# Optimization experiments

Hardware: AMD Instinct MI355X
Metric: run time of the kernel (lower is better)

Reference implementation:

```python
import jax, jax.numpy as jnp
import numpy as np

VOCAB, D, H, L, SEQ = 32000, 768, 12, 6, 1024
HD = D // H
DFF = 4 * D
EPS = 1e-5


def _ln(x, g, b):
    mu = jnp.mean(x, axis=-1, keepdims=True)
    var = jnp.var(x, axis=-1, keepdims=True)
    return (x - mu) * jax.lax.rsqrt(var + EPS) * g + b


def setup_inputs() -> dict:
    key = jax.random.key(0)
    ks = jax.random.split(key, 10)
    s = lambda *sh: 0.02
    return {
        "idx": jax.random.randint(ks[0], (2, SEQ), 0, VOCAB, dtype=jnp.int64) if jax.config.jax_enable_x64 else jax.random.randint(ks[0], (2, SEQ), 0, VOCAB, dtype=jnp.int32),
        "tok_emb": jax.random.normal(ks[1], (VOCAB, D), jnp.float32) * 0.02,
        "pos_emb": jax.random.normal(ks[2], (SEQ, D), jnp.float32) * 0.02,
        "Wqkv": jax.random.normal(ks[3], (L, D, 3 * D), jnp.float32) * 0.02,
        "bqkv": jnp.zeros((L, 3 * D), jnp.float32),
        "Wo": jax.random.normal(ks[4], (L, D, D), jnp.float32) * 0.02,
        "bo": jnp.zeros((L, D), jnp.float32),
        "ln1_g": jnp.ones((L, D), jnp.float32),
        "ln1_b": jnp.zeros((L, D), jnp.float32),
        "ln2_g": jnp.ones((L, D), jnp.float32),
        "ln2_b": jnp.zeros((L, D), jnp.float32),
        "W1": jax.random.normal(ks[5], (L, D, DFF), jnp.float32) * 0.02,
        "b1": jnp.zeros((L, DFF), jnp.float32),
        "W2": jax.random.normal(ks[6], (L, DFF, D), jnp.float32) * 0.02,
        "b2": jnp.zeros((L, D), jnp.float32),
        "lnf_g": jnp.ones((D,), jnp.float32),
        "lnf_b": jnp.zeros((D,), jnp.float32),
        "Wlm": jax.random.normal(ks[7], (D, VOCAB), jnp.float32) * 0.02,
    }


def _forward(idx, tok_emb, pos_emb, Wqkv, bqkv, Wo, bo, ln1_g, ln1_b,
             ln2_g, ln2_b, W1, b1, W2, b2, lnf_g, lnf_b, Wlm):
    B, T = idx.shape
    x = tok_emb[idx] + pos_emb[None, :T]  # [B,T,D]
    causal = jnp.tril(jnp.ones((T, T), bool))  # [T,T]
    for l in range(L):
        h = _ln(x, ln1_g[l], ln1_b[l])
        qkv = h @ Wqkv[l] + bqkv[l]  # [B,T,3D]
        qkv = qkv.reshape(B, T, 3, H, HD).transpose(2, 0, 3, 1, 4)
        q, k, v = qkv[0], qkv[1], qkv[2]  # each [B,H,T,HD]
        att = jnp.einsum('bhqd,bhkd->bhqk', q, k) / np.sqrt(HD).astype(np.float32)
        att = jnp.where(causal, att, -jnp.inf)
        att = jax.nn.softmax(att, axis=-1)
        o = jnp.einsum('bhqk,bhkd->bhqd', att, v)
        o = o.transpose(0, 2, 1, 3).reshape(B, T, D)
        x = x + o @ Wo[l] + bo[l]
        h = _ln(x, ln2_g[l], ln2_b[l])
        x = x + jax.nn.gelu(h @ W1[l] + b1[l], approximate=False) @ W2[l] + b2[l]
    x = _ln(x, lnf_g, lnf_b)
    return x @ Wlm  # [B,T,VOCAB]


def reference(idx, tok_emb, pos_emb, Wqkv, bqkv, Wo, bo, ln1_g, ln1_b,
              ln2_g, ln2_b, W1, b1, W2, b2, lnf_g, lnf_b, Wlm):
    return _forward(idx, tok_emb, pos_emb, Wqkv, bqkv, Wo, bo, ln1_g, ln1_b,
                    ln2_g, ln2_b, W1, b1, W2, b2, lnf_g, lnf_b, Wlm)
```

## Files before the change

kernel.cpp:

```cpp
#include <hip/hip_runtime.h>
#include <math.h>

#define TT   1024
#define DD   768
#define HH   12
#define LLAY 6
#define DFFN 3072
#define BB   2
#define NTOK (BB*TT)

typedef __bf16 bf16;
typedef __attribute__((ext_vector_type(8))) __bf16 bf16x8;
typedef __attribute__((ext_vector_type(4))) __bf16 bf16x4;
typedef __attribute__((ext_vector_type(4))) float f32x4;

__device__ inline unsigned pack_bf16x2(float a, float b) {
    union { bf16 h[2]; unsigned u; } un;
    un.h[0] = (bf16)a; un.h[1] = (bf16)b;
    return un.u;
}

__device__ inline void gload16(const bf16* g, bf16* l) {
    __builtin_amdgcn_global_load_lds((const void*)g, (void*)l, 16, 0, 0);
}

template<int N> __device__ inline void waitcnt_vm() {
    if constexpr (N == 0) asm volatile("s_waitcnt vmcnt(0)" ::: "memory");
    else if constexpr (N == 3) asm volatile("s_waitcnt vmcnt(3)" ::: "memory");
    else if constexpr (N == 4) asm volatile("s_waitcnt vmcnt(4)" ::: "memory");
}

__global__ __launch_bounds__(256) void embed_kernel(const int* __restrict__ idx,
                                                    const float* __restrict__ tok,
                                                    const float* __restrict__ pos,
                                                    float* __restrict__ x) {
    int bt = blockIdx.x;
    int t  = bt % TT;
    int id = idx[bt];
    const float* te = tok + (size_t)id * DD;
    const float* pe = pos + (size_t)t * DD;
    float* xr = x + (size_t)bt * DD;
    for (int d = threadIdx.x; d < DD; d += 256) xr[d] = te[d] + pe[d];
}

__global__ __launch_bounds__(256) void ln_kernel(const float* __restrict__ in,
                                                 const float* __restrict__ g,
                                                 const float* __restrict__ b,
                                                 bf16* __restrict__ out) {
    int row = blockIdx.x;
    const float* xr = in + (size_t)row * DD;
    float s = 0.f, s2 = 0.f;
    for (int d = threadIdx.x; d < DD; d += 256) { float v = xr[d]; s += v; s2 += v * v; }
    for (int off = 32; off; off >>= 1) { s += __shfl_down(s, off); s2 += __shfl_down(s2, off); }
    __shared__ float aS[4], aS2[4];
    __shared__ float mu_s, rs_s;
    int wid = threadIdx.x >> 6, lane = threadIdx.x & 63;
    if (lane == 0) { aS[wid] = s; aS2[wid] = s2; }
    __syncthreads();
    if (threadIdx.x == 0) {
        float t1 = aS[0] + aS[1] + aS[2] + aS[3];
        float t2 = aS2[0] + aS2[1] + aS2[2] + aS2[3];
        float mu = t1 / (float)DD;
        float var = t2 / (float)DD - mu * mu;
        mu_s = mu; rs_s = rsqrtf(var + 1e-5f);
    }
    __syncthreads();
    float mu = mu_s, rs = rs_s;
    bf16* orow = out + (size_t)row * DD;
    for (int d = threadIdx.x; d < DD; d += 256)
        orow[d] = (bf16)((xr[d] - mu) * rs * g[d] + b[d]);
}

__device__ inline void convT_tile(const float* __restrict__ in, bf16* __restrict__ out,
                                  int K, int N, int k0, int n0) {
    __shared__ float tile[32][33];
    int tn = threadIdx.x & 31, tk = threadIdx.x >> 5;
#pragma unroll
    for (int i = 0; i < 4; ++i)
        tile[tk + i * 8][tn] = in[(size_t)(k0 + tk + i * 8) * N + n0 + tn];
    __syncthreads();
#pragma unroll
    for (int i = 0; i < 4; ++i)
        out[(size_t)(n0 + tk + i * 8) * K + k0 + tn] = (bf16)tile[tn][tk + i * 8];
}

__global__ __launch_bounds__(256) void convT_kernel(const float* __restrict__ in,
                                                    bf16* __restrict__ out,
                                                    int K, int N) {
    convT_tile(in, out, K, N, blockIdx.y * 32, blockIdx.x * 32);
}

__global__ __launch_bounds__(256) void convT4_kernel(const float* __restrict__ w0,
                                                     const float* __restrict__ w1,
                                                     const float* __restrict__ w2,
                                                     const float* __restrict__ w3,
                                                     bf16* __restrict__ o0,
                                                     bf16* __restrict__ o1,
                                                     bf16* __restrict__ o2,
                                                     bf16* __restrict__ o3) {
    int bid = blockIdx.x;
    const float* in; bf16* out; int K, N, t;
    if (bid < 1728)      { in = w0; out = o0; K = 768;  N = 2304; t = bid; }
    else if (bid < 2304) { in = w1; out = o1; K = 768;  N = 768;  t = bid - 1728; }
    else if (bid < 4608) { in = w2; out = o2; K = 768;  N = 3072; t = bid - 2304; }
    else                 { in = w3; out = o3; K = 3072; N = 768;  t = bid - 4608; }
    int nt = N / 32;
    convT_tile(in, out, K, N, (t / nt) * 32, (t % nt) * 32);
}

template<int BM, int EPI>
__global__ __launch_bounds__(256) void mgemm(const bf16* __restrict__ A,
                                             const bf16* __restrict__ Bt,
                                             const float* __restrict__ bias,
                                             const float* __restrict__ res,
                                             void* __restrict__ Cout,
                                             bf16* __restrict__ vtout,
                                             int M, int N, int K) {
    constexpr int MF = BM / 32;
    constexpr int NF = 4;
    constexpr int AIT = BM / 64;
    constexpr int STG = AIT + 2;
    constexpr int ASZ = BM * 32;
    constexpr int BUFE = ASZ + 128 * 32;
    __shared__ __align__(16) bf16 smem[3 * BUFE];
    int bm = blockIdx.y * BM;
    int bn = blockIdx.x * 128;
    int tid = threadIdx.x;
    int lane = tid & 63;
    int w = tid >> 6;
    int wr = w >> 1, wc = w & 1;
    int l15 = lane & 15, g = lane >> 4;

    f32x4 acc[MF][NF];
#pragma unroll
    for (int m = 0; m < MF; ++m)
#pragma unroll
        for (int n = 0; n < NF; ++n) acc[m][n] = (f32x4){0.f, 0.f, 0.f, 0.f};

    int r = lane >> 2;
    int koff = ((lane & 3) ^ ((r >> 1) & 3)) * 8;
    const bf16* Ab = A + (size_t)(bm + w * 16 + r) * K + koff;
    const bf16* Bb = Bt + (size_t)(bn + w * 16 + r) * K + koff;

    auto stage = [&](int p, int k0) {
        bf16* base = smem + p * BUFE;
        bf16* Asb = base + w * 16 * 32;
        bf16* Bsb = base + ASZ + w * 16 * 32;
#pragma unroll
        for (int it = 0; it < AIT; ++it)
            gload16(Ab + (size_t)(it * 64) * K + k0, Asb + it * 64 * 32);
#pragma unroll
        for (int it = 0; it < 2; ++it)
            gload16(Bb + (size_t)(it * 64) * K + k0, Bsb + it * 64 * 32);
    };

    stage(0, 0);
    stage(1, 32);
    waitcnt_vm<STG>();
    __builtin_amdgcn_s_barrier();
    int cur = 0;

    for (int k0 = 0; k0 < K; k0 += 32) {
        const bf16* Ac = smem + cur * BUFE;
        const bf16* Bc = Ac + ASZ;
        bf16x8 af[MF], bfv[NF];
#pragma unroll
        for (int m = 0; m < MF; ++m) {
            int row = wr * (BM / 2) + m * 16 + l15;
            int gs = g ^ ((row >> 1) & 3);
            af[m] = *(const bf16x8*)&Ac[row * 32 + gs * 8];
        }
#pragma unroll
        for (int n = 0; n < NF; ++n) {
            int row = wc * 64 + n * 16 + l15;
            int gs = g ^ ((row >> 1) & 3);
            bfv[n] = *(const bf16x8*)&Bc[row * 32 + gs * 8];
        }
        bool st = (k0 + 64 < K);
        if (st) {
            int nxt = cur + 2; if (nxt >= 3) nxt -= 3;
            stage(nxt, k0 + 64);
        }
#pragma unroll
        for (int m = 0; m < MF; ++m)
#pragma unroll
            for (int n = 0; n < NF; ++n)
                acc[m][n] = __builtin_amdgcn_mfma_f32_16x16x32_bf16(af[m], bfv[n], acc[m][n], 0, 0, 0);
        if (st) waitcnt_vm<STG>();
        else    waitcnt_vm<0>();
        __builtin_amdgcn_s_barrier();
        cur = (cur == 2) ? 0 : cur + 1;
    }

    int lq = g * 4;
#pragma unroll
    for (int m = 0; m < MF; ++m) {
#pragma unroll
        for (int n = 0; n < NF; ++n) {
            int col = bn + wc * 64 + n * 16 + l15;
            float bv = bias[col];
            if (EPI == 4 && col >= 2 * DD) {
                int row0 = bm + wr * (BM / 2) + m * 16 + lq;
                int b = row0 >> 10, t0 = row0 & 1023;
                int hd = col - 2 * DD;
                union { bf16 h[4]; unsigned long long u; } pk;
#pragma unroll
                for (int j = 0; j < 4; ++j) pk.h[j] = (bf16)(acc[m][n][j] + bv);
                *(unsigned long long*)&vtout[((size_t)(b * DD + hd)) * TT + t0] = pk.u;
            } else {
#pragma unroll
                for (int j = 0; j < 4; ++j) {
                    int row = bm + wr * (BM / 2) + m * 16 + lq + j;
                    float v = acc[m][n][j] + bv;
                    if (EPI == 2) {
                        ((float*)Cout)[(size_t)row * N + col] = v + res[(size_t)row * N + col];
                    } else if (EPI == 3) {
                        v = 0.5f * v * (1.f + erff(v * 0.70710678118654752f));
                        ((bf16*)Cout)[(size_t)row * N + col] = (bf16)v;
                    } else if (EPI == 1) {
                        ((bf16*)Cout)[(size_t)row * N + col] = (bf16)v;
                    } else {
                        if (col < DD) v *= 0.125f;
                        ((bf16*)Cout)[(size_t)row * N + col] = (bf16)v;
                    }
                }
            }
        }
    }
}

__global__ __launch_bounds__(512, 2) void lmgemm(const bf16* __restrict__ A,
                                                 const bf16* __restrict__ Bt,
                                                 float* __restrict__ C) {
    constexpr int BUFE = 2 * 256 * 64;
    __shared__ __align__(16) bf16 smem[2 * BUFE];
    const int tid = threadIdx.x;
    const int w = tid >> 6, lane = tid & 63;
    const int wm = w >> 2, wn = w & 3;
    const int l15 = lane & 15, g = lane >> 4;
    const int bm = blockIdx.x * 256;
    const int bn = blockIdx.y * 256;

    const int swzr = (l15 >> 1) & 7;
    const int pc0 = (g ^ swzr) * 8;

    const int r8 = lane >> 3, c8 = lane & 7;
    const bf16* agp[4]; const bf16* bgp[4];
    int aldso[4], bldso[4];
#pragma unroll
    for (int j = 0; j < 4; ++j) {
        int br = w * 32 + j * 8 + r8;
        int swz = (br >> 1) & 7;
        agp[j] = A  + (size_t)(bm + br) * DD + (c8 ^ swz) * 8;
        bgp[j] = Bt + (size_t)(bn + br) * DD + (c8 ^ swz) * 8;
        aldso[j] = (w * 32 + j * 8) * 64;
        bldso[j] = 256 * 64 + (w * 32 + j * 8) * 64;
    }

    f32x4 acc[8][4];
#pragma unroll
    for (int m = 0; m < 8; ++m)
#pragma unroll
        for (int n = 0; n < 4; ++n) acc[m][n] = (f32x4){0.f, 0.f, 0.f, 0.f};

    {
        bf16* base = smem;
#pragma unroll
        for (int j = 0; j < 4; ++j) gload16(agp[j], base + aldso[j]);
#pragma unroll
        for (int j = 0; j < 4; ++j) gload16(bgp[j], base + bldso[j]);
    }
    __syncthreads();
    int cur = 0;

    for (int t = 0; t < 12; ++t) {
        const bf16* Ar = smem + cur * BUFE;
        const bf16* Br = Ar + 256 * 64;
        bf16* nbase = smem + (cur ^ 1) * BUFE;
        const int k0n = (t + 1) * 64;
        const bool st = (t < 11);
        if (st) {
#pragma unroll
            for (int j = 0; j < 4; ++j) gload16(agp[j] + k0n, nbase + aldso[j]);
        }
        bf16x8 af[8], bfv[4];
#pragma unroll
        for (int m = 0; m < 8; ++m)
            af[m] = *(const bf16x8*)&Ar[(wm * 128 + m * 16 + l15) * 64 + pc0];
#pragma unroll
        for (int n = 0; n < 4; ++n)
            bfv[n] = *(const bf16x8*)&Br[(wn * 64 + n * 16 + l15) * 64 + pc0];
        __builtin_amdgcn_s_setprio(1);
#pragma unroll
        for (int m = 0; m < 8; ++m)
#pragma unroll
            for (int n = 0; n < 4; ++n)
                acc[m][n] = __builtin_amdgcn_mfma_f32_16x16x32_bf16(af[m], bfv[n], acc[m][n], 0, 0, 0);
        __builtin_amdgcn_s_setprio(0);
        if (st) {
#pragma unroll
            for (int j = 0; j < 4; ++j) gload16(bgp[j] + k0n, nbase + bldso[j]);
        }
#pragma unroll
        for (int m = 0; m < 8; ++m)
            af[m] = *(const bf16x8*)&Ar[(wm * 128 + m * 16 + l15) * 64 + (pc0 ^ 32)];
#pragma unroll
        for (int n = 0; n < 4; ++n)
            bfv[n] = *(const bf16x8*)&Br[(wn * 64 + n * 16 + l15) * 64 + (pc0 ^ 32)];
        __builtin_amdgcn_s_setprio(1);
#pragma unroll
        for (int m = 0; m < 8; ++m)
#pragma unroll
            for (int n = 0; n < 4; ++n)
                acc[m][n] = __builtin_amdgcn_mfma_f32_16x16x32_bf16(af[m], bfv[n], acc[m][n], 0, 0, 0);
        __builtin_amdgcn_s_setprio(0);
        __syncthreads();
        cur ^= 1;
    }

    float* eb = (float*)smem + w * (16 * 68);
    const int rr = lane >> 2, c0 = (lane & 3) * 16;
#pragma unroll
    for (int mf = 0; mf < 8; ++mf) {
#pragma unroll
        for (int n = 0; n < 4; ++n)
#pragma unroll
            for (int j = 0; j < 4; ++j)
                eb[(g * 4 + j) * 68 + n * 16 + l15] = acc[mf][n][j];
        __syncthreads();
        const float* src = &eb[rr * 68 + c0];
        float* dst = C + (size_t)(bm + wm * 128 + mf * 16 + rr) * 32000 + bn + wn * 64 + c0;
        *(float4*)(dst + 0)  = *(const float4*)(src + 0);
        *(float4*)(dst + 4)  = *(const float4*)(src + 4);
        *(float4*)(dst + 8)  = *(const float4*)(src + 8);
        *(float4*)(dst + 12) = *(const float4*)(src + 12);
        __syncthreads();
    }
}

__global__ __launch_bounds__(256) void fattn_kernel(const bf16* __restrict__ qkv,
                                                    const bf16* __restrict__ vt,
                                                    bf16* __restrict__ o) {
    const int bh = blockIdx.y;
    const int b = bh / HH, h = bh % HH;
    const int q0 = blockIdx.x * 64;
    const int tid = threadIdx.x;
    const int w = tid >> 6, lane = tid & 63;
    const int l15 = lane & 15, g = lane >> 4;

    __shared__ __align__(16) bf16 Ks[64 * 64];
    __shared__ __align__(16) bf16 Vs[64 * 64];
    __shared__ __align__(16) bf16 Ps[4][16 * 64];

    const size_t basebt = (size_t)b * TT;
    const int qw = q0 + w * 16;
    const int qg = qw + l15;

    bf16x8 bq0, bq1;
    {
        const bf16* qp = qkv + (basebt + qw + l15) * 2304 + h * 64 + g * 8;
        bq0 = *(const bf16x8*)(qp);
        bq1 = *(const bf16x8*)(qp + 32);
    }

    float mstate = -1e30f, lstate = 0.f;
    f32x4 oacc[4];
#pragma unroll
    for (int nf = 0; nf < 4; ++nf) oacc[nf] = (f32x4){0.f, 0.f, 0.f, 0.f};

    const int swzA = (l15 & 7) << 4;
    char* const psBase = (char*)&Ps[w][0];

    const int nchunk = blockIdx.x + 1;
    for (int c = 0; c < nchunk; ++c) {
        const int kc = c * 64;
        __syncthreads();
        {
            int r0 = tid >> 3;
            int e0 = (tid & 7) * 8;
#pragma unroll
            for (int i = 0; i < 2; ++i) {
                int r = r0 + 32 * i;
                int swzW = (r & 7) << 4;
                bf16x8 kv = *(const bf16x8*)&qkv[(basebt + kc + r) * 2304 + DD + h * 64 + e0];
                *(bf16x8*)((char*)Ks + r * 128 + ((e0 * 2) ^ swzW)) = kv;
                bf16x8 vv = *(const bf16x8*)&vt[((size_t)bh * 64 + r) * TT + kc + e0];
                *(bf16x8*)((char*)Vs + r * 128 + ((e0 * 2) ^ swzW)) = vv;
            }
        }
        __syncthreads();
        if (kc > qw + 15) continue;

        f32x4 s[4];
        __builtin_amdgcn_s_setprio(1);
#pragma unroll
        for (int mf = 0; mf < 4; ++mf) {
            char* kr = (char*)Ks + (16 * mf + l15) * 128;
            bf16x8 ka0 = *(const bf16x8*)(kr + ((16 * g) ^ swzA));
            bf16x8 ka1 = *(const bf16x8*)(kr + ((64 + 16 * g) ^ swzA));
            f32x4 a = (f32x4){0.f, 0.f, 0.f, 0.f};
            a = __builtin_amdgcn_mfma_f32_16x16x32_bf16(ka0, bq0, a, 0, 0, 0);
            a = __builtin_amdgcn_mfma_f32_16x16x32_bf16(ka1, bq1, a, 0, 0, 0);
            s[mf] = a;
        }
        __builtin_amdgcn_s_setprio(0);
        if (kc + 63 > qw) {
#pragma unroll
            for (int mf = 0; mf < 4; ++mf)
#pragma unroll
                for (int j = 0; j < 4; ++j)
                    if (kc + 16 * mf + 4 * g + j > qg) s[mf][j] = -1e30f;
        }
        float cm = -1e30f;
#pragma unroll
        for (int mf = 0; mf < 4; ++mf)
#pragma unroll
            for (int j = 0; j < 4; ++j) cm = fmaxf(cm, s[mf][j]);
        cm = fmaxf(cm, __shfl_xor(cm, 16));
        cm = fmaxf(cm, __shfl_xor(cm, 32));
        float mnew = fmaxf(mstate, cm);
        float sc = __expf(mstate - mnew);
        mstate = mnew;
        float p[4][4];
        float psum = 0.f;
#pragma unroll
        for (int mf = 0; mf < 4; ++mf)
#pragma unroll
            for (int j = 0; j < 4; ++j) { float pv = __expf(s[mf][j] - mnew); p[mf][j] = pv; psum += pv; }
        psum += __shfl_xor(psum, 16);
        psum += __shfl_xor(psum, 32);
        lstate = lstate * sc + psum;
#pragma unroll
        for (int mf = 0; mf < 4; ++mf) {
            unsigned lo = pack_bf16x2(p[mf][0], p[mf][1]);
            unsigned hi = pack_bf16x2(p[mf][2], p[mf][3]);
            char* dst = psBase + l15 * 128 + ((32 * mf + 8 * g) ^ swzA);
            *(unsigned*)dst = lo;
            *(unsigned*)(dst + 4) = hi;
        }
        float s0 = __shfl(sc, 4 * g + 0), s1 = __shfl(sc, 4 * g + 1);
        float s2 = __shfl(sc, 4 * g + 2), s3 = __shfl(sc, 4 * g + 3);
#pragma unroll
        for (int nf = 0; nf < 4; ++nf) {
            oacc[nf][0] *= s0; oacc[nf][1] *= s1; oacc[nf][2] *= s2; oacc[nf][3] *= s3;
        }
        bf16x8 pa0 = *(const bf16x8*)(psBase + l15 * 128 + ((16 * g) ^ swzA));
        bf16x8 pa1 = *(const bf16x8*)(psBase + l15 * 128 + ((64 + 16 * g) ^ swzA));
        __builtin_amdgcn_s_setprio(1);
#pragma unroll
        for (int nf = 0; nf < 4; ++nf) {
            char* vr = (char*)Vs + (16 * nf + l15) * 128;
            bf16x8 vb0 = *(const bf16x8*)(vr + ((16 * g) ^ swzA));
            bf16x8 vb1 = *(const bf16x8*)(vr + ((64 + 16 * g) ^ swzA));
            oacc[nf] = __builtin_amdgcn_mfma_f32_16x16x32_bf16(pa0, vb0, oacc[nf], 0, 0, 0);
            oacc[nf] = __builtin_amdgcn_mfma_f32_16x16x32_bf16(pa1, vb1, oacc[nf], 0, 0, 0);
        }
        __builtin_amdgcn_s_setprio(0);
    }
    float linv = 1.f / lstate;
    float l0 = __shfl(linv, 4 * g + 0), l1 = __shfl(linv, 4 * g + 1);
    float l2 = __shfl(linv, 4 * g + 2), l3 = __shfl(linv, 4 * g + 3);
    float lj[4] = {l0, l1, l2, l3};
#pragma unroll
    for (int j = 0; j < 4; ++j) {
        bf16* orow = o + (size_t)(basebt + qw + 4 * g + j) * DD + h * 64 + l15;
#pragma unroll
        for (int nf = 0; nf < 4; ++nf)
            orow[16 * nf] = (bf16)(oacc[nf][j] * lj[j]);
    }
}

extern "C" void kernel_launch(void* const* d_in, const int* in_sizes, int n_in,
                              void* d_out, int out_size, void* d_ws, size_t ws_size,
                              hipStream_t stream) {
    (void)in_sizes; (void)n_in; (void)out_size; (void)ws_size;
    const int*   idx  = (const int*)d_in[0];
    const float* tok  = (const float*)d_in[1];
    const float* pos  = (const float*)d_in[2];
    const float* Wqkv = (const float*)d_in[3];
    const float* bqkv = (const float*)d_in[4];
    const float* Wo   = (const float*)d_in[5];
    const float* bo   = (const float*)d_in[6];
    const float* ln1g = (const float*)d_in[7];
    const float* ln1b = (const float*)d_in[8];
    const float* ln2g = (const float*)d_in[9];
    const float* ln2b = (const float*)d_in[10];
    const float* W1   = (const float*)d_in[11];
    const float* b1   = (const float*)d_in[12];
    const float* W2   = (const float*)d_in[13];
    const float* b2   = (const float*)d_in[14];
    const float* lnfg = (const float*)d_in[15];
    const float* lnfb = (const float*)d_in[16];
    const float* Wlm  = (const float*)d_in[17];
    float* out = (float*)d_out;

    char* ws = (char*)d_ws;
    float* x     = (float*)(ws);
    bf16*  abuf0 = (bf16*)(ws + 6291456);
    bf16*  abuf1 = (bf16*)(ws + 9437184);
    bf16*  qkvb  = (bf16*)(ws + 22020096);
    bf16*  vtb   = (bf16*)(ws + 31457280);
    bf16*  wbuf  = (bf16*)(ws + 34603008);

    bf16* wq = wbuf;
    bf16* wo = wbuf + 1769472;
    bf16* w1 = wbuf + 2359296;
    bf16* w2 = wbuf + 4718592;

    embed_kernel<<<NTOK, 256, 0, stream>>>(idx, tok, pos, x);

    for (int l = 0; l < LLAY; ++l) {
        convT4_kernel<<<6912, 256, 0, stream>>>(
            Wqkv + (size_t)l * DD * 3 * DD, Wo + (size_t)l * DD * DD,
            W1 + (size_t)l * DD * DFFN, W2 + (size_t)l * DFFN * DD,
            wq, wo, w1, w2);
        ln_kernel<<<NTOK, 256, 0, stream>>>(x, ln1g + l * DD, ln1b + l * DD, abuf0);
        mgemm<128, 4><<<dim3(3 * DD / 128, NTOK / 128), 256, 0, stream>>>(
            abuf0, wq, bqkv + (size_t)l * 3 * DD, nullptr, qkvb, vtb, NTOK, 3 * DD, DD);
        fattn_kernel<<<dim3(TT / 64, BB * HH), 256, 0, stream>>>(qkvb, vtb, abuf0);
        mgemm<64, 2><<<dim3(DD / 128, NTOK / 64), 256, 0, stream>>>(
            abuf0, wo, bo + (size_t)l * DD, x, x, nullptr, NTOK, DD, DD);
        ln_kernel<<<NTOK, 256, 0, stream>>>(x, ln2g + l * DD, ln2b + l * DD, abuf0);
        mgemm<128, 3><<<dim3(DFFN / 128, NTOK / 128), 256, 0, stream>>>(
            abuf0, w1, b1 + (size_t)l * DFFN, nullptr, abuf1, nullptr, NTOK, DFFN, DD);
        mgemm<64, 2><<<dim3(DD / 128, NTOK / 64), 256, 0, stream>>>(
            abuf1, w2, b2 + (size_t)l * DD, x, x, nullptr, NTOK, DD, DFFN);
    }
    ln_kernel<<<NTOK, 256, 0, stream>>>(x, lnfg, lnfb, abuf0);
    convT_kernel<<<dim3(32000 / 32, DD / 32), 256, 0, stream>>>(Wlm, wbuf, DD, 32000);
    lmgemm<<<dim3(NTOK / 256, 32000 / 256), 512, 0, stream>>>(abuf0, wbuf, out);
}
```

Before: 1.008 ms.

## Deepen LM-head GEMM pipeline, wave-per-row layernorm, reverse attention block order

The LM-head GEMM moves from a two-buffer pipeline with K-step 64 to a four-buffer pipeline with K-step 32. Three stages stay in flight, gated by vmcnt waits and raw barriers, so global-to-LDS loads overlap the MFMA work. Layernorm now gives each wavefront one row, using float4 loads and a shuffle reduction in place of shared-memory block reductions and syncthreads. Flash attention launches the longest causal query blocks first to balance load across the tail. The deeper pipeline uses more LDS and changes the swizzle, which could affect occupancy or cause bank conflicts.

```diff
diff --git a/kernel.cpp b/kernel.cpp
--- a/kernel.cpp
+++ b/kernel.cpp
@@ -28,6 +28,7 @@
     if constexpr (N == 0) asm volatile("s_waitcnt vmcnt(0)" ::: "memory");
     else if constexpr (N == 3) asm volatile("s_waitcnt vmcnt(3)" ::: "memory");
     else if constexpr (N == 4) asm volatile("s_waitcnt vmcnt(4)" ::: "memory");
+    else if constexpr (N == 8) asm volatile("s_waitcnt vmcnt(8)" ::: "memory");
 }
 
 __global__ __launch_bounds__(256) void embed_kernel(const int* __restrict__ idx,
@@ -47,28 +48,33 @@
                                                  const float* __restrict__ g,
                                                  const float* __restrict__ b,
                                                  bf16* __restrict__ out) {
-    int row = blockIdx.x;
+    const int wid = threadIdx.x >> 6, lane = threadIdx.x & 63;
+    const int row = blockIdx.x * 4 + wid;
     const float* xr = in + (size_t)row * DD;
+    float4 v[3];
     float s = 0.f, s2 = 0.f;
-    for (int d = threadIdx.x; d < DD; d += 256) { float v = xr[d]; s += v; s2 += v * v; }
+#pragma unroll
+    for (int j = 0; j < 3; ++j) {
+        v[j] = *(const float4*)&xr[lane * 4 + 256 * j];
+        s  += v[j].x + v[j].y + v[j].z + v[j].w;
+        s2 += v[j].x * v[j].x + v[j].y * v[j].y + v[j].z * v[j].z + v[j].w * v[j].w;
+    }
     for (int off = 32; off; off >>= 1) { s += __shfl_down(s, off); s2 += __shfl_down(s2, off); }
-    __shared__ float aS[4], aS2[4];
-    __shared__ float mu_s, rs_s;
-    int wid = threadIdx.x >> 6, lane = threadIdx.x & 63;
-    if (lane == 0) { aS[wid] = s; aS2[wid] = s2; }
-    __syncthreads();
-    if (threadIdx.x == 0) {
-        float t1 = aS[0] + aS[1] + aS[2] + aS[3];
-        float t2 = aS2[0] + aS2[1] + aS2[2] + aS2[3];
-        float mu = t1 / (float)DD;
-        float var = t2 / (float)DD - mu * mu;
-        mu_s = mu; rs_s = rsqrtf(var + 1e-5f);
-    }
-    __syncthreads();
-    float mu = mu_s, rs = rs_s;
+    s = __shfl(s, 0); s2 = __shfl(s2, 0);
+    const float mu = s / (float)DD;
+    const float rs = rsqrtf(s2 / (float)DD - mu * mu + 1e-5f);
     bf16* orow = out + (size_t)row * DD;
-    for (int d = threadIdx.x; d < DD; d += 256)
-        orow[d] = (bf16)((xr[d] - mu) * rs * g[d] + b[d]);
+#pragma unroll
+    for (int j = 0; j < 3; ++j) {
+        float4 gg = *(const float4*)&g[lane * 4 + 256 * j];
+        float4 bb = *(const float4*)&b[lane * 4 + 256 * j];
+        bf16x4 o;
+        o[0] = (bf16)((v[j].x - mu) * rs * gg.x + bb.x);
+        o[1] = (bf16)((v[j].y - mu) * rs * gg.y + bb.y);
+        o[2] = (bf16)((v[j].z - mu) * rs * gg.z + bb.z);
+        o[3] = (bf16)((v[j].w - mu) * rs * gg.w + bb.w);
+        *(bf16x4*)&orow[lane * 4 + 256 * j] = o;
+    }
 }
 
 __device__ inline void convT_tile(const float* __restrict__ in, bf16* __restrict__ out,
@@ -232,8 +238,9 @@
 __global__ __launch_bounds__(512, 2) void lmgemm(const bf16* __restrict__ A,
                                                  const bf16* __restrict__ Bt,
                                                  float* __restrict__ C) {
-    constexpr int BUFE = 2 * 256 * 64;
-    __shared__ __align__(16) bf16 smem[2 * BUFE];
+    constexpr int ABUF = 256 * 32;
+    constexpr int BUFE = 2 * ABUF;
+    __shared__ __align__(16) bf16 smem[4 * BUFE];
     const int tid = threadIdx.x;
     const int w = tid >> 6, lane = tid & 63;
     const int wm = w >> 2, wn = w & 3;
@@ -241,21 +248,14 @@
     const int bm = blockIdx.x * 256;
     const int bn = blockIdx.y * 256;
 
-    const int swzr = (l15 >> 1) & 7;
-    const int pc0 = (g ^ swzr) * 8;
-
-    const int r8 = lane >> 3, c8 = lane & 7;
-    const bf16* agp[4]; const bf16* bgp[4];
-    int aldso[4], bldso[4];
-#pragma unroll
-    for (int j = 0; j < 4; ++j) {
-        int br = w * 32 + j * 8 + r8;
-        int swz = (br >> 1) & 7;
-        agp[j] = A  + (size_t)(bm + br) * DD + (c8 ^ swz) * 8;
-        bgp[j] = Bt + (size_t)(bn + br) * DD + (c8 ^ swz) * 8;
-        aldso[j] = (w * 32 + j * 8) * 64;
-        bldso[j] = 256 * 64 + (w * 32 + j * 8) * 64;
-    }
+    const int fcol = ((g ^ ((l15 >> 1) & 3))) * 8;
+
+    const int rA = lane >> 2;
+    const int csw = ((lane & 3) ^ ((lane >> 3) & 3)) * 8;
+    const bf16* a0 = A  + (size_t)(bm + w * 16 + rA) * DD + csw;
+    const bf16* b0 = Bt + (size_t)(bn + w * 16 + rA) * DD + csw;
+    const int ld0 = (w * 16) * 32;
+    const int ld1 = (w * 16 + 128) * 32;
 
     f32x4 acc[8][4];
 #pragma unroll
@@ -263,33 +263,31 @@
 #pragma unroll
         for (int n = 0; n < 4; ++n) acc[m][n] = (f32x4){0.f, 0.f, 0.f, 0.f};
 
-    {
-        bf16* base = smem;
-#pragma unroll
-        for (int j = 0; j < 4; ++j) gload16(agp[j], base + aldso[j]);
-#pragma unroll
-        for (int j = 0; j < 4; ++j) gload16(bgp[j], base + bldso[j]);
-    }
-    __syncthreads();
-    int cur = 0;
-
-    for (int t = 0; t < 12; ++t) {
-        const bf16* Ar = smem + cur * BUFE;
-        const bf16* Br = Ar + 256 * 64;
-        bf16* nbase = smem + (cur ^ 1) * BUFE;
-        const int k0n = (t + 1) * 64;
-        const bool st = (t < 11);
-        if (st) {
-#pragma unroll
-            for (int j = 0; j < 4; ++j) gload16(agp[j] + k0n, nbase + aldso[j]);
-        }
+    auto stagef = [&](int p, int kelem) {
+        bf16* base = smem + p * BUFE;
+        gload16(a0 + kelem, base + ld0);
+        gload16(a0 + (size_t)128 * DD + kelem, base + ld1);
+        gload16(b0 + kelem, base + ABUF + ld0);
+        gload16(b0 + (size_t)128 * DD + kelem, base + ABUF + ld1);
+    };
+
+    stagef(0, 0);
+    stagef(1, 32);
+    stagef(2, 64);
+    waitcnt_vm<8>();
+    __builtin_amdgcn_s_barrier();
+
+    for (int t = 0; t < 21; ++t) {
+        const bf16* Ar = smem + (t & 3) * BUFE;
+        const bf16* Br = Ar + ABUF;
         bf16x8 af[8], bfv[4];
 #pragma unroll
         for (int m = 0; m < 8; ++m)
-            af[m] = *(const bf16x8*)&Ar[(wm * 128 + m * 16 + l15) * 64 + pc0];
+            af[m] = *(const bf16x8*)&Ar[(wm * 128 + m * 16 + l15) * 32 + fcol];
 #pragma unroll
         for (int n = 0; n < 4; ++n)
-            bfv[n] = *(const bf16x8*)&Br[(wn * 64 + n * 16 + l15) * 64 + pc0];
+            bfv[n] = *(const bf16x8*)&Br[(wn * 64 + n * 16 + l15) * 32 + fcol];
+        stagef((t + 3) & 3, (t + 3) * 32);
         __builtin_amdgcn_s_setprio(1);
 #pragma unroll
         for (int m = 0; m < 8; ++m)
@@ -297,27 +295,30 @@
             for (int n = 0; n < 4; ++n)
                 acc[m][n] = __builtin_amdgcn_mfma_f32_16x16x32_bf16(af[m], bfv[n], acc[m][n], 0, 0, 0);
         __builtin_amdgcn_s_setprio(0);
-        if (st) {
-#pragma unroll
-            for (int j = 0; j < 4; ++j) gload16(bgp[j] + k0n, nbase + bldso[j]);
-        }
+        waitcnt_vm<8>();
+        __builtin_amdgcn_s_barrier();
+    }
+    waitcnt_vm<0>();
+    __builtin_amdgcn_s_barrier();
+#pragma unroll
+    for (int t = 21; t < 24; ++t) {
+        const bf16* Ar = smem + (t & 3) * BUFE;
+        const bf16* Br = Ar + ABUF;
+        bf16x8 af[8], bfv[4];
 #pragma unroll
         for (int m = 0; m < 8; ++m)
-            af[m] = *(const bf16x8*)&Ar[(wm * 128 + m * 16 + l15) * 64 + (pc0 ^ 32)];
+            af[m] = *(const bf16x8*)&Ar[(wm * 128 + m * 16 + l15) * 32 + fcol];
 #pragma unroll
         for (int n = 0; n < 4; ++n)
-            bfv[n] = *(const bf16x8*)&Br[(wn * 64 + n * 16 + l15) * 64 + (pc0 ^ 32)];
-        __builtin_amdgcn_s_setprio(1);
+            bfv[n] = *(const bf16x8*)&Br[(wn * 64 + n * 16 + l15) * 32 + fcol];
 #pragma unroll
         for (int m = 0; m < 8; ++m)
 #pragma unroll
             for (int n = 0; n < 4; ++n)
                 acc[m][n] = __builtin_amdgcn_mfma_f32_16x16x32_bf16(af[m], bfv[n], acc[m][n], 0, 0, 0);
-        __builtin_amdgcn_s_setprio(0);
-        __syncthreads();
-        cur ^= 1;
-    }
-
+    }
+
+    __syncthreads();
     float* eb = (float*)smem + w * (16 * 68);
     const int rr = lane >> 2, c0 = (lane & 3) * 16;
 #pragma unroll
@@ -343,7 +344,8 @@
                                                     bf16* __restrict__ o) {
     const int bh = blockIdx.y;
     const int b = bh / HH, h = bh % HH;
-    const int q0 = blockIdx.x * 64;
+    const int qc = gridDim.x - 1 - blockIdx.x;
+    const int q0 = qc * 64;
     const int tid = threadIdx.x;
     const int w = tid >> 6, lane = tid & 63;
     const int l15 = lane & 15, g = lane >> 4;
@@ -371,7 +373,7 @@
     const int swzA = (l15 & 7) << 4;
     char* const psBase = (char*)&Ps[w][0];
 
-    const int nchunk = blockIdx.x + 1;
+    const int nchunk = qc + 1;
     for (int c = 0; c < nchunk; ++c) {
         const int kc = c * 64;
         __syncthreads();
@@ -514,19 +516,19 @@
             Wqkv + (size_t)l * DD * 3 * DD, Wo + (size_t)l * DD * DD,
             W1 + (size_t)l * DD * DFFN, W2 + (size_t)l * DFFN * DD,
             wq, wo, w1, w2);
-        ln_kernel<<<NTOK, 256, 0, stream>>>(x, ln1g + l * DD, ln1b + l * DD, abuf0);
+        ln_kernel<<<NTOK / 4, 256, 0, stream>>>(x, ln1g + l * DD, ln1b + l * DD, abuf0);
         mgemm<128, 4><<<dim3(3 * DD / 128, NTOK / 128), 256, 0, stream>>>(
             abuf0, wq, bqkv + (size_t)l * 3 * DD, nullptr, qkvb, vtb, NTOK, 3 * DD, DD);
         fattn_kernel<<<dim3(TT / 64, BB * HH), 256, 0, stream>>>(qkvb, vtb, abuf0);
         mgemm<64, 2><<<dim3(DD / 128, NTOK / 64), 256, 0, stream>>>(
             abuf0, wo, bo + (size_t)l * DD, x, x, nullptr, NTOK, DD, DD);
-        ln_kernel<<<NTOK, 256, 0, stream>>>(x, ln2g + l * DD, ln2b + l * DD, abuf0);
+        ln_kernel<<<NTOK / 4, 256, 0, stream>>>(x, ln2g + l * DD, ln2b + l * DD, abuf0);
         mgemm<128, 3><<<dim3(DFFN / 128, NTOK / 128), 256, 0, stream>>>(
             abuf0, w1, b1 + (size_t)l * DFFN, nullptr, abuf1, nullptr, NTOK, DFFN, DD);
         mgemm<64, 2><<<dim3(DD / 128, NTOK / 64), 256, 0, stream>>>(
             abuf1, w2, b2 + (size_t)l * DD, x, x, nullptr, NTOK, DD, DFFN);
     }
-    ln_kernel<<<NTOK, 256, 0, stream>>>(x, lnfg, lnfb, abuf0);
+    ln_kernel<<<NTOK / 4, 256, 0, stream>>>(x, lnfg, lnfb, abuf0);
     convT_kernel<<<dim3(32000 / 32, DD / 32), 256, 0, stream>>>(Wlm, wbuf, DD, 32000);
     lmgemm<<<dim3(NTOK / 256, 32000 / 256), 512, 0, stream>>>(abuf0, wbuf, out);
 }
```

Result: no change. 1.005 ms (-0.3%).

## Vectorize layernorm per-wave, enlarge transpose tiles, remap LM-head blocks, reverse attention order

Applied to the files above, without the earlier changes.

Layernorm now handles one row per wavefront with float4 loads and shuffle reductions, removing shared-memory reductions and block syncs. Weight transposes use 64x64 tiles with fewer blocks. The LM-head GEMM uses a 1D grid remapped so each XCD processes contiguous vocab column blocks for L2 reuse, with out-of-range blocks exiting early. Causal attention launches the heaviest query blocks first to reduce tail imbalance.

```diff
diff --git a/kernel.cpp b/kernel.cpp
--- a/kernel.cpp
+++ b/kernel.cpp
@@ -47,47 +47,52 @@
                                                  const float* __restrict__ g,
                                                  const float* __restrict__ b,
                                                  bf16* __restrict__ out) {
-    int row = blockIdx.x;
+    const int wid = threadIdx.x >> 6, lane = threadIdx.x & 63;
+    const int row = blockIdx.x * 4 + wid;
     const float* xr = in + (size_t)row * DD;
+    float4 v[3];
     float s = 0.f, s2 = 0.f;
-    for (int d = threadIdx.x; d < DD; d += 256) { float v = xr[d]; s += v; s2 += v * v; }
+#pragma unroll
+    for (int j = 0; j < 3; ++j) {
+        v[j] = *(const float4*)&xr[lane * 4 + 256 * j];
+        s  += v[j].x + v[j].y + v[j].z + v[j].w;
+        s2 += v[j].x * v[j].x + v[j].y * v[j].y + v[j].z * v[j].z + v[j].w * v[j].w;
+    }
     for (int off = 32; off; off >>= 1) { s += __shfl_down(s, off); s2 += __shfl_down(s2, off); }
-    __shared__ float aS[4], aS2[4];
-    __shared__ float mu_s, rs_s;
-    int wid = threadIdx.x >> 6, lane = threadIdx.x & 63;
-    if (lane == 0) { aS[wid] = s; aS2[wid] = s2; }
+    s = __shfl(s, 0); s2 = __shfl(s2, 0);
+    const float mu = s / (float)DD;
+    const float rs = rsqrtf(s2 / (float)DD - mu * mu + 1e-5f);
+    bf16* orow = out + (size_t)row * DD;
+#pragma unroll
+    for (int j = 0; j < 3; ++j) {
+        float4 gg = *(const float4*)&g[lane * 4 + 256 * j];
+        float4 bb = *(const float4*)&b[lane * 4 + 256 * j];
+        bf16x4 o;
+        o[0] = (bf16)((v[j].x - mu) * rs * gg.x + bb.x);
+        o[1] = (bf16)((v[j].y - mu) * rs * gg.y + bb.y);
+        o[2] = (bf16)((v[j].z - mu) * rs * gg.z + bb.z);
+        o[3] = (bf16)((v[j].w - mu) * rs * gg.w + bb.w);
+        *(bf16x4*)&orow[lane * 4 + 256 * j] = o;
+    }
+}
+
+__device__ inline void convT_tile64(const float* __restrict__ in, bf16* __restrict__ out,
+                                    int K, int N, int k0, int n0) {
+    __shared__ float tile[64][65];
+    const int c = threadIdx.x & 63, q = threadIdx.x >> 6;
+#pragma unroll
+    for (int i = 0; i < 16; ++i)
+        tile[q + i * 4][c] = in[(size_t)(k0 + q + i * 4) * N + n0 + c];
     __syncthreads();
-    if (threadIdx.x == 0) {
-        float t1 = aS[0] + aS[1] + aS[2] + aS[3];
-        float t2 = aS2[0] + aS2[1] + aS2[2] + aS2[3];
-        float mu = t1 / (float)DD;
-        float var = t2 / (float)DD - mu * mu;
-        mu_s = mu; rs_s = rsqrtf(var + 1e-5f);
-    }
-    __syncthreads();
-    float mu = mu_s, rs = rs_s;
-    bf16* orow = out + (size_t)row * DD;
-    for (int d = threadIdx.x; d < DD; d += 256)
-        orow[d] = (bf16)((xr[d] - mu) * rs * g[d] + b[d]);
-}
-
-__device__ inline void convT_tile(const float* __restrict__ in, bf16* __restrict__ out,
-                                  int K, int N, int k0, int n0) {
-    __shared__ float tile[32][33];
-    int tn = threadIdx.x & 31, tk = threadIdx.x >> 5;
-#pragma unroll
-    for (int i = 0; i < 4; ++i)
-        tile[tk + i * 8][tn] = in[(size_t)(k0 + tk + i * 8) * N + n0 + tn];
-    __syncthreads();
-#pragma unroll
-    for (int i = 0; i < 4; ++i)
-        out[(size_t)(n0 + tk + i * 8) * K + k0 + tn] = (bf16)tile[tn][tk + i * 8];
+#pragma unroll
+    for (int i = 0; i < 16; ++i)
+        out[(size_t)(n0 + q + i * 4) * K + k0 + c] = (bf16)tile[c][q + i * 4];
 }
 
 __global__ __launch_bounds__(256) void convT_kernel(const float* __restrict__ in,
                                                     bf16* __restrict__ out,
                                                     int K, int N) {
-    convT_tile(in, out, K, N, blockIdx.y * 32, blockIdx.x * 32);
+    convT_tile64(in, out, K, N, blockIdx.y * 64, blockIdx.x * 64);
 }
 
 __global__ __launch_bounds__(256) void convT4_kernel(const float* __restrict__ w0,
@@ -100,12 +105,12 @@
                                                      bf16* __restrict__ o3) {
     int bid = blockIdx.x;
     const float* in; bf16* out; int K, N, t;
-    if (bid < 1728)      { in = w0; out = o0; K = 768;  N = 2304; t = bid; }
-    else if (bid < 2304) { in = w1; out = o1; K = 768;  N = 768;  t = bid - 1728; }
-    else if (bid < 4608) { in = w2; out = o2; K = 768;  N = 3072; t = bid - 2304; }
-    else                 { in = w3; out = o3; K = 3072; N = 768;  t = bid - 4608; }
-    int nt = N / 32;
-    convT_tile(in, out, K, N, (t / nt) * 32, (t % nt) * 32);
+    if (bid < 432)       { in = w0; out = o0; K = 768;  N = 2304; t = bid; }
+    else if (bid < 576)  { in = w1; out = o1; K = 768;  N = 768;  t = bid - 432; }
+    else if (bid < 1152) { in = w2; out = o2; K = 768;  N = 3072; t = bid - 576; }
+    else                 { in = w3; out = o3; K = 3072; N = 768;  t = bid - 1152; }
+    int nt = N / 64;
+    convT_tile64(in, out, K, N, (t / nt) * 64, (t % nt) * 64);
 }
 
 template<int BM, int EPI>
@@ -234,12 +239,16 @@
                                                  float* __restrict__ C) {
     constexpr int BUFE = 2 * 256 * 64;
     __shared__ __align__(16) bf16 smem[2 * BUFE];
+    const int orig = blockIdx.x;
+    const int xcd = orig & 7, local = orig >> 3;
+    const int bnb = xcd * 16 + (local >> 3);
+    if (bnb >= 125) return;
+    const int bm = (local & 7) * 256;
+    const int bn = bnb * 256;
     const int tid = threadIdx.x;
     const int w = tid >> 6, lane = tid & 63;
     const int wm = w >> 2, wn = w & 3;
     const int l15 = lane & 15, g = lane >> 4;
-    const int bm = blockIdx.x * 256;
-    const int bn = blockIdx.y * 256;
 
     const int swzr = (l15 >> 1) & 7;
     const int pc0 = (g ^ swzr) * 8;
@@ -343,7 +352,8 @@
                                                     bf16* __restrict__ o) {
     const int bh = blockIdx.y;
     const int b = bh / HH, h = bh % HH;
-    const int q0 = blockIdx.x * 64;
+    const int qc = gridDim.x - 1 - blockIdx.x;
+    const int q0 = qc * 64;
     const int tid = threadIdx.x;
     const int w = tid >> 6, lane = tid & 63;
     const int l15 = lane & 15, g = lane >> 4;
@@ -371,7 +381,7 @@
     const int swzA = (l15 & 7) << 4;
     char* const psBase = (char*)&Ps[w][0];
 
-    const int nchunk = blockIdx.x + 1;
+    const int nchunk = qc + 1;
     for (int c = 0; c < nchunk; ++c) {
         const int kc = c * 64;
         __syncthreads();
@@ -510,23 +520,23 @@
     embed_kernel<<<NTOK, 256, 0, stream>>>(idx, tok, pos, x);
 
     for (int l = 0; l < LLAY; ++l) {
-        convT4_kernel<<<6912, 256, 0, stream>>>(
+        convT4_kernel<<<1728, 256, 0, stream>>>(
             Wqkv + (size_t)l * DD * 3 * DD, Wo + (size_t)l * DD * DD,
             W1 + (size_t)l * DD * DFFN, W2 + (size_t)l * DFFN * DD,
             wq, wo, w1, w2);
-        ln_kernel<<<NTOK, 256, 0, stream>>>(x, ln1g + l * DD, ln1b + l * DD, abuf0);
+        ln_kernel<<<NTOK / 4, 256, 0, stream>>>(x, ln1g + l * DD, ln1b + l * DD, abuf0);
         mgemm<128, 4><<<dim3(3 * DD / 128, NTOK / 128), 256, 0, stream>>>(
             abuf0, wq, bqkv + (size_t)l * 3 * DD, nullptr, qkvb, vtb, NTOK, 3 * DD, DD);
         fattn_kernel<<<dim3(TT / 64, BB * HH), 256, 0, stream>>>(qkvb, vtb, abuf0);
         mgemm<64, 2><<<dim3(DD / 128, NTOK / 64), 256, 0, stream>>>(
             abuf0, wo, bo + (size_t)l * DD, x, x, nullptr, NTOK, DD, DD);
-        ln_kernel<<<NTOK, 256, 0, stream>>>(x, ln2g + l * DD, ln2b + l * DD, abuf0);
+        ln_kernel<<<NTOK / 4, 256, 0, stream>>>(x, ln2g + l * DD, ln2b + l * DD, abuf0);
         mgemm<128, 3><<<dim3(DFFN / 128, NTOK / 128), 256, 0, stream>>>(
             abuf0, w1, b1 + (size_t)l * DFFN, nullptr, abuf1, nullptr, NTOK, DFFN, DD);
         mgemm<64, 2><<<dim3(DD / 128, NTOK / 64), 256, 0, stream>>>(
             abuf1, w2, b2 + (size_t)l * DD, x, x, nullptr, NTOK, DD, DFFN);
     }
-    ln_kernel<<<NTOK, 256, 0, stream>>>(x, lnfg, lnfb, abuf0);
-    convT_kernel<<<dim3(32000 / 32, DD / 32), 256, 0, stream>>>(Wlm, wbuf, DD, 32000);
-    lmgemm<<<dim3(NTOK / 256, 32000 / 256), 512, 0, stream>>>(abuf0, wbuf, out);
-}
+    ln_kernel<<<NTOK / 4, 256, 0, stream>>>(x, lnfg, lnfb, abuf0);
+    convT_kernel<<<dim3(32000 / 64, DD / 64), 256, 0, stream>>>(Wlm, wbuf, DD, 32000);
+    lmgemm<<<1024, 512, 0, stream>>>(abuf0, wbuf, out);
+}
```

After: 995.1 us. No clear change (-1.3%).
